# Kernel optimization log

Measured on AMD Instinct MI355X. Metric: run time of the kernel, lower is better.

The kernel has to match this reference:

```python
import jax, jax.numpy as jnp
import numpy as np

EPS_GUMBEL = 1e-20
EPS_LOG = 1e-10
N = 16384


def setup_inputs() -> dict:
    key = jax.random.key(0)
    k1, k2 = jax.random.split(key)
    logits = jax.random.normal(k1, (N,), dtype=jnp.float32)
    u = jax.random.uniform(k2, (N,), dtype=jnp.float32)
    # same transform as torch sample_gumbel
    gumbel_noise = -jnp.log(-jnp.log(u + EPS_GUMBEL) + EPS_GUMBEL)
    return {"logits": logits, "gumbel_noise": gumbel_noise}


def reference(logits, gumbel_noise):
    # gumbel-perturbed logits (training path, is_evaluate=False)
    g = logits + gumbel_noise                      # [n]
    # rank_mask[i, j] = g[i] >= g[j]
    rank_mask = g[:, None] >= g[None, :]           # [n, n] bool
    # rd[i, j] = exp(logits[j] - logits[i]) where mask else 0
    rd = jnp.where(rank_mask,
                   jnp.exp(logits[None, :] - logits[:, None]),
                   jnp.float32(0.0))               # [n, n]
    log_prob = -jnp.log(rd.sum(axis=1) + EPS_LOG)  # [n]
    return (log_prob, g)
```

## Files before the change

kernel.cpp:

```cpp
#include <hip/hip_runtime.h>


#define EPS_LOG 1e-10f

constexpr int TPB    = 256;
constexpr int IPT    = 8;
constexpr int IBLK   = TPB * IPT;
constexpr int JCHUNK = 256;


__global__ __launch_bounds__(TPB) void gs_partial(const float* __restrict__ logits,
                                                  const float* __restrict__ noise,
                                                  float* __restrict__ partial,
                                                  int n) {
    __shared__ float2 tile[JCHUNK];
    const int ib = blockIdx.x;
    const int jc = blockIdx.y;
    const int jbase = jc * JCHUNK;

    for (int t = threadIdx.x; t < JCHUNK; t += TPB) {
        float l = logits[jbase + t];
        tile[t] = make_float2(l + noise[jbase + t], __expf(l));
    }

    const int i0 = ib * IBLK + (int)threadIdx.x;
    float gi[IPT];
    #pragma unroll
    for (int k = 0; k < IPT; ++k) {
        int i = i0 + k * TPB;
        gi[k] = logits[i] + noise[i];
    }
    __syncthreads();

    float s[IPT];
    #pragma unroll
    for (int k = 0; k < IPT; ++k) s[k] = 0.0f;

    #pragma unroll 4
    for (int j = 0; j < JCHUNK; ++j) {
        float2 t = tile[j];
        #pragma unroll
        for (int k = 0; k < IPT; ++k)
            s[k] += (t.x <= gi[k]) ? t.y : 0.0f;
    }

    #pragma unroll
    for (int k = 0; k < IPT; ++k)
        partial[(size_t)jc * n + i0 + k * TPB] = s[k];
}

__global__ __launch_bounds__(TPB) void gs_finalize(const float* __restrict__ partial,
                                                   const float* __restrict__ logits,
                                                   const float* __restrict__ noise,
                                                   float* __restrict__ out,
                                                   int n, int n_jchunks) {
    int i = blockIdx.x * TPB + threadIdx.x;
    if (i >= n) return;
    float s = 0.0f;
    for (int c = 0; c < n_jchunks; ++c)
        s += partial[(size_t)c * n + i];
    float l = logits[i];
    out[i]     = -__logf(s * __expf(-l) + EPS_LOG);
    out[n + i] = l + noise[i];
}

extern "C" void kernel_launch(void* const* d_in, const int* in_sizes, int n_in,
                              void* d_out, int out_size, void* d_ws, size_t ws_size,
                              hipStream_t stream) {
    const float* logits = (const float*)d_in[0];
    const float* noise  = (const float*)d_in[1];
    float* out = (float*)d_out;
    const int n = in_sizes[0];

    float* partial = (float*)d_ws;

    const int n_iblocks = (n + IBLK - 1) / IBLK;
    const int n_jchunks = (n + JCHUNK - 1) / JCHUNK;

    dim3 grid(n_iblocks, n_jchunks);
    gs_partial<<<grid, TPB, 0, stream>>>(logits, noise, partial, n);
    gs_finalize<<<(n + TPB - 1) / TPB, TPB, 0, stream>>>(partial, logits, noise, out, n, n_jchunks);
}
```

Before: 93.66 us.

## Replace quadratic rank-mask sum with bucketed prefix sums over perturbed logits

Instead of comparing every pair, elements are scattered into fixed-width buckets keyed by perturbed logit, with per-bucket exp sums accumulated atomically. A scan produces prefix sums of lower buckets, and each element scans only its own bucket for exact comparisons. This removes the O(n^2) compare work at the cost of several launches, atomics, and a fixed bucket range and capacity that could drop entries if a bucket overflows.

```diff
diff --git a/kernel.cpp b/kernel.cpp
--- a/kernel.cpp
+++ b/kernel.cpp
@@ -3,65 +3,89 @@
 
 #define EPS_LOG 1e-10f
 
-constexpr int TPB    = 256;
-constexpr int IPT    = 8;
-constexpr int IBLK   = TPB * IPT;
-constexpr int JCHUNK = 256;
+constexpr int   TPB    = 256;
+constexpr int   NBKT   = 2048;
+constexpr int   MAXPB  = 1024;
+constexpr float G_LO   = -32.0f;
+constexpr float G_INVW = 32.0f;
 
 
-__global__ __launch_bounds__(TPB) void gs_partial(const float* __restrict__ logits,
-                                                  const float* __restrict__ noise,
-                                                  float* __restrict__ partial,
-                                                  int n) {
-    __shared__ float2 tile[JCHUNK];
-    const int ib = blockIdx.x;
-    const int jc = blockIdx.y;
-    const int jbase = jc * JCHUNK;
-
-    for (int t = threadIdx.x; t < JCHUNK; t += TPB) {
-        float l = logits[jbase + t];
-        tile[t] = make_float2(l + noise[jbase + t], __expf(l));
-    }
-
-    const int i0 = ib * IBLK + (int)threadIdx.x;
-    float gi[IPT];
-    #pragma unroll
-    for (int k = 0; k < IPT; ++k) {
-        int i = i0 + k * TPB;
-        gi[k] = logits[i] + noise[i];
-    }
-    __syncthreads();
-
-    float s[IPT];
-    #pragma unroll
-    for (int k = 0; k < IPT; ++k) s[k] = 0.0f;
-
-    #pragma unroll 4
-    for (int j = 0; j < JCHUNK; ++j) {
-        float2 t = tile[j];
-        #pragma unroll
-        for (int k = 0; k < IPT; ++k)
-            s[k] += (t.x <= gi[k]) ? t.y : 0.0f;
-    }
-
-    #pragma unroll
-    for (int k = 0; k < IPT; ++k)
-        partial[(size_t)jc * n + i0 + k * TPB] = s[k];
+__device__ __forceinline__ int bucket_of(float g) {
+    int b = (int)((g - G_LO) * G_INVW);
+    return min(max(b, 0), NBKT - 1);
 }
 
-__global__ __launch_bounds__(TPB) void gs_finalize(const float* __restrict__ partial,
-                                                   const float* __restrict__ logits,
-                                                   const float* __restrict__ noise,
-                                                   float* __restrict__ out,
-                                                   int n, int n_jchunks) {
+__global__ __launch_bounds__(TPB) void gs_zero(int* __restrict__ cnt,
+                                               float* __restrict__ esum) {
+    int t = blockIdx.x * TPB + threadIdx.x;
+    if (t < NBKT) { cnt[t] = 0; esum[t] = 0.0f; }
+}
+
+__global__ __launch_bounds__(TPB) void gs_scatter(const float* __restrict__ logits,
+                                                  const float* __restrict__ noise,
+                                                  int* __restrict__ cnt,
+                                                  float* __restrict__ esum,
+                                                  float2* __restrict__ slots,
+                                                  float* __restrict__ g_out,
+                                                  int n) {
     int i = blockIdx.x * TPB + threadIdx.x;
     if (i >= n) return;
+    float l = logits[i];
+    float g = l + noise[i];
+    g_out[i] = g;
+    float e = __expf(l);
+    int b = bucket_of(g);
+    atomicAdd(&esum[b], e);
+    int slot = atomicAdd(&cnt[b], 1);
+    if (slot < MAXPB)
+        slots[(size_t)b * MAXPB + slot] = make_float2(g, e);
+}
+
+__global__ __launch_bounds__(64) void gs_scan(const float* __restrict__ esum,
+                                              float* __restrict__ epre) {
+    int t = threadIdx.x;
+    float loc[32];
     float s = 0.0f;
-    for (int c = 0; c < n_jchunks; ++c)
-        s += partial[(size_t)c * n + i];
+    #pragma unroll
+    for (int k = 0; k < 32; ++k) {
+        loc[k] = esum[t * 32 + k];
+        s += loc[k];
+    }
+    float x = s;
+    #pragma unroll
+    for (int off = 1; off < 64; off <<= 1) {
+        float v = __shfl_up(x, off, 64);
+        if (t >= off) x += v;
+    }
+    float running = x - s;
+    #pragma unroll
+    for (int k = 0; k < 32; ++k) {
+        epre[t * 32 + k] = running;
+        running += loc[k];
+    }
+}
+
+__global__ __launch_bounds__(TPB) void gs_final(const float* __restrict__ logits,
+                                                const float* __restrict__ noise,
+                                                const int* __restrict__ cnt,
+                                                const float* __restrict__ epre,
+                                                const float2* __restrict__ slots,
+                                                float* __restrict__ out,
+                                                int n) {
+    int i = blockIdx.x * TPB + threadIdx.x;
+    if (i >= n) return;
     float l = logits[i];
-    out[i]     = -__logf(s * __expf(-l) + EPS_LOG);
-    out[n + i] = l + noise[i];
+    float g = l + noise[i];
+    int b = bucket_of(g);
+    int c = min(cnt[b], MAXPB);
+    const float2* __restrict__ row = slots + (size_t)b * MAXPB;
+    float S = 0.0f;
+    #pragma unroll 4
+    for (int k = 0; k < c; ++k) {
+        float2 ge = row[k];
+        S += (ge.x <= g) ? ge.y : 0.0f;
+    }
+    out[i] = -__logf((epre[b] + S) * __expf(-l) + EPS_LOG);
 }
 
 extern "C" void kernel_launch(void* const* d_in, const int* in_sizes, int n_in,
@@ -72,12 +96,16 @@
     float* out = (float*)d_out;
     const int n = in_sizes[0];
 
-    float* partial = (float*)d_ws;
+    char* ws = (char*)d_ws;
+    int*    cnt   = (int*)ws;
+    float*  esum  = (float*)(ws + (size_t)NBKT * 4);
+    float*  epre  = (float*)(ws + (size_t)NBKT * 8);
+    float2* slots = (float2*)(ws + (size_t)NBKT * 16);
 
-    const int n_iblocks = (n + IBLK - 1) / IBLK;
-    const int n_jchunks = (n + JCHUNK - 1) / JCHUNK;
-
-    dim3 grid(n_iblocks, n_jchunks);
-    gs_partial<<<grid, TPB, 0, stream>>>(logits, noise, partial, n);
-    gs_finalize<<<(n + TPB - 1) / TPB, TPB, 0, stream>>>(partial, logits, noise, out, n, n_jchunks);
+    gs_zero   <<<(NBKT + TPB - 1) / TPB, TPB, 0, stream>>>(cnt, esum);
+    gs_scatter<<<(n + TPB - 1) / TPB, TPB, 0, stream>>>(logits, noise, cnt, esum,
+                                                        slots, out + n, n);
+    gs_scan   <<<1, 64, 0, stream>>>(esum, epre);
+    gs_final  <<<(n + TPB - 1) / TPB, TPB, 0, stream>>>(logits, noise, cnt, epre,
+                                                        slots, out, n);
 }
```

Result: faster. 84.12 us (-10.2%).
